# Performance work log

Hardware: AMD Instinct MI355X
Metric: run time of the kernel (lower is better)

Reference implementation:

```python
import jax, jax.numpy as jnp
import numpy as np

N = 50000
E = 800000
IN_CH = 64
HID = 128
K1 = 64
K2 = 16
THR = 1.0 / (K1 - 1)
EPS_LN = 1e-5


def setup_inputs() -> dict:
    key = jax.random.key(0)
    ks = jax.random.split(key, 10)
    def w(k, shape):
        return jax.random.normal(k, shape, jnp.float32) / np.sqrt(shape[0]).astype(np.float32)
    return {
        "x": jax.random.normal(ks[0], (N, IN_CH), jnp.float32),
        "edge_index": jax.random.randint(ks[1], (2, E), 0, N),
        "W1_rel": w(ks[2], (IN_CH, HID)),
        "b1_rel": jnp.zeros((HID,), jnp.float32),
        "W1_root": w(ks[3], (IN_CH, HID)),
        "Wp1": w(ks[4], (HID, K1)),
        "bp1": jnp.zeros((K1,), jnp.float32),
        "ln1_w": jnp.ones((K1,), jnp.float32),
        "ln1_b": jnp.zeros((K1,), jnp.float32),
        "W2_rel": w(ks[5], (HID, HID)),
        "b2_rel": jnp.zeros((HID,), jnp.float32),
        "W2_root": w(ks[6], (HID, HID)),
        "Wp2": w(ks[7], (HID, K2)),
        "bp2": jnp.zeros((K2,), jnp.float32),
        "ln2_w": jnp.ones((K2,), jnp.float32),
        "ln2_b": jnp.zeros((K2,), jnp.float32),
    }


def _layer_norm(x, w, b):
    m = x.mean(-1, keepdims=True)
    v = ((x - m) ** 2).mean(-1, keepdims=True)
    return (x - m) / jnp.sqrt(v + EPS_LN) * w + b


def _mincut_core(x, s, A_s, deg):
    # s already softmaxed. A_s[i] = sum_j A[i,j] s[j]; deg[i] = sum_j A[i,j].
    k = s.shape[1]
    pooled_x = s.T @ x                       # [k, F]
    pooled_adj = s.T @ A_s                   # [k, k]
    mincut_num = jnp.trace(pooled_adj)
    mincut_den = jnp.trace(s.T @ (deg[:, None] * s)) + 1e-10
    mincut_loss = -mincut_num / mincut_den
    sT_s = s.T @ s
    nrm = jnp.linalg.norm(sT_s)
    eye = jnp.eye(k, dtype=s.dtype)
    ortho_loss = jnp.linalg.norm(sT_s / (nrm + 1e-10) - eye / np.sqrt(k).astype(np.float32))
    adj = pooled_adj * (1.0 - eye)           # zero diagonal
    d_sqrt = jnp.sqrt(adj.sum(1))[:, None]
    inv = 1.0 / (d_sqrt + 1e-15)
    adj_norm = adj * inv * inv.T
    return pooled_x, adj_norm, mincut_loss, ortho_loss


def _forward(x, edge_index, W1_rel, b1_rel, W1_root, Wp1, bp1, ln1_w, ln1_b,
             W2_rel, b2_rel, W2_root, Wp2, bp2, ln2_w, ln2_b):
    n = x.shape[0]
    src, dst = edge_index[0], edge_index[1]
    # GraphConv 1: sum-aggregate source features at target, then linear + root
    agg1 = jax.ops.segment_sum(x[src], dst, num_segments=n)
    x1 = jax.nn.relu(agg1 @ W1_rel + b1_rel + x @ W1_root)
    s1 = _layer_norm(x1 @ Wp1 + bp1, ln1_w, ln1_b)
    s1_soft = jax.nn.softmax(s1, axis=-1)
    # sparse mincut pool 1 (edge list, unit weights): A_s[row] += s[col]
    A_s1 = jax.ops.segment_sum(s1_soft[src], src * 0 + src, num_segments=n) if False else jax.ops.segment_sum(s1_soft[dst], src, num_segments=n)
    deg1 = jax.ops.segment_sum(jnp.ones((E,), x.dtype), src, num_segments=n)
    x_pool1, adj1, mc1, o1 = _mincut_core(x1, s1_soft, A_s1, deg1)
    # threshold -> binary coarse adjacency (replaces torch nonzero edge list)
    A1 = jnp.where(adj1 > THR, 1.0, 0.0).astype(x.dtype)    # [K1, K1]
    # GraphConv 2 on dense binary A1 (edges (r,c): message x[r] -> node c)
    agg2 = A1.T @ x_pool1
    x2 = jax.nn.relu(agg2 @ W2_rel + b2_rel + x_pool1 @ W2_root)
    s2 = _layer_norm(x2 @ Wp2 + bp2, ln2_w, ln2_b)
    s2_soft = jax.nn.softmax(s2, axis=-1)
    A_s2 = A1 @ s2_soft
    deg2 = A1.sum(1)
    _, adj2, mc2, o2 = _mincut_core(x2, s2_soft, A_s2, deg2)
    return (mc1, o1, mc2, o2, s1, A1, s2, adj2)


def reference(x, edge_index, W1_rel, b1_rel, W1_root, Wp1, bp1, ln1_w, ln1_b,
              W2_rel, b2_rel, W2_root, Wp2, bp2, ln2_w, ln2_b):
    return _forward(x, edge_index, W1_rel, b1_rel, W1_root, Wp1, bp1, ln1_w, ln1_b,
                    W2_rel, b2_rel, W2_root, Wp2, bp2, ln2_w, ln2_b)
```

## Files before the change

kernel.cpp:

```cpp
#include <hip/hip_runtime.h>

#define NN 50000
#define EE 800000
#define NT32 1563
#define NTILE 3125
#define NSB 196
#define MAXSLAB 512

#define OUT_S1 4
#define OUT_A1 (4 + NN * 64)
#define OUT_S2 (OUT_A1 + 64 * 64)
#define OUT_ADJ2 (OUT_S2 + 64 * 16)

__device__ __forceinline__ float block_sum256(float v, float* red) {
  v += __shfl_xor(v, 32); v += __shfl_xor(v, 16); v += __shfl_xor(v, 8);
  v += __shfl_xor(v, 4);  v += __shfl_xor(v, 2);  v += __shfl_xor(v, 1);
  __syncthreads();
  if ((threadIdx.x & 63) == 0) red[threadIdx.x >> 6] = v;
  __syncthreads();
  return red[0] + red[1] + red[2] + red[3];
}

__device__ __forceinline__ float4 gather_rows64(
    const float* __restrict__ rows, const int* __restrict__ csr,
    int off, int c, int l, int g) {
  float4 a0 = make_float4(0.f, 0.f, 0.f, 0.f);
  float4 a1 = a0, a2 = a0, a3 = a0;
  int bb = 0;
  for (; bb + 16 <= c; bb += 16) {
    int myid = csr[off + bb + l];
    #pragma unroll
    for (int j = 0; j < 16; j += 4) {
      int s0 = __shfl(myid, g + j + 0, 64);
      int s1 = __shfl(myid, g + j + 1, 64);
      int s2 = __shfl(myid, g + j + 2, 64);
      int s3 = __shfl(myid, g + j + 3, 64);
      const float4 v0 = *(const float4*)&rows[(size_t)s0 * 64 + l * 4];
      const float4 v1 = *(const float4*)&rows[(size_t)s1 * 64 + l * 4];
      const float4 v2 = *(const float4*)&rows[(size_t)s2 * 64 + l * 4];
      const float4 v3 = *(const float4*)&rows[(size_t)s3 * 64 + l * 4];
      a0.x += v0.x; a0.y += v0.y; a0.z += v0.z; a0.w += v0.w;
      a1.x += v1.x; a1.y += v1.y; a1.z += v1.z; a1.w += v1.w;
      a2.x += v2.x; a2.y += v2.y; a2.z += v2.z; a2.w += v2.w;
      a3.x += v3.x; a3.y += v3.y; a3.z += v3.z; a3.w += v3.w;
    }
  }
  int m = c - bb;
  if (m > 0) {
    int myid = (l < m) ? csr[off + bb + l] : 0;
    int j = 0;
    for (; j + 2 <= m; j += 2) {
      int s0 = __shfl(myid, g + j + 0, 64);
      int s1 = __shfl(myid, g + j + 1, 64);
      const float4 v0 = *(const float4*)&rows[(size_t)s0 * 64 + l * 4];
      const float4 v1 = *(const float4*)&rows[(size_t)s1 * 64 + l * 4];
      a0.x += v0.x; a0.y += v0.y; a0.z += v0.z; a0.w += v0.w;
      a1.x += v1.x; a1.y += v1.y; a1.z += v1.z; a1.w += v1.w;
    }
    if (j < m) {
      int s0 = __shfl(myid, g + j, 64);
      const float4 v0 = *(const float4*)&rows[(size_t)s0 * 64 + l * 4];
      a2.x += v0.x; a2.y += v0.y; a2.z += v0.z; a2.w += v0.w;
    }
  }
  a0.x += a1.x; a0.y += a1.y; a0.z += a1.z; a0.w += a1.w;
  a2.x += a3.x; a2.y += a3.y; a2.z += a3.z; a2.w += a3.w;
  a0.x += a2.x; a0.y += a2.y; a0.z += a2.z; a0.w += a2.w;
  return a0;
}

__device__ __forceinline__ float4 gather_rows64_sq(
    const float* __restrict__ rows, const int* __restrict__ csr,
    int off, int c, int l, int g, float& dsq) {
  float4 a0 = make_float4(0.f, 0.f, 0.f, 0.f);
  float4 a1 = a0, a2 = a0, a3 = a0;
  int bb = 0;
  for (; bb + 16 <= c; bb += 16) {
    int myid = csr[off + bb + l];
    #pragma unroll
    for (int j = 0; j < 16; j += 4) {
      int s0 = __shfl(myid, g + j + 0, 64);
      int s1 = __shfl(myid, g + j + 1, 64);
      int s2 = __shfl(myid, g + j + 2, 64);
      int s3 = __shfl(myid, g + j + 3, 64);
      const float4 v0 = *(const float4*)&rows[(size_t)s0 * 64 + l * 4];
      const float4 v1 = *(const float4*)&rows[(size_t)s1 * 64 + l * 4];
      const float4 v2 = *(const float4*)&rows[(size_t)s2 * 64 + l * 4];
      const float4 v3 = *(const float4*)&rows[(size_t)s3 * 64 + l * 4];
      a0.x += v0.x; a0.y += v0.y; a0.z += v0.z; a0.w += v0.w;
      a1.x += v1.x; a1.y += v1.y; a1.z += v1.z; a1.w += v1.w;
      a2.x += v2.x; a2.y += v2.y; a2.z += v2.z; a2.w += v2.w;
      a3.x += v3.x; a3.y += v3.y; a3.z += v3.z; a3.w += v3.w;
      dsq += v0.x * v0.x + v0.y * v0.y + v0.z * v0.z + v0.w * v0.w;
      dsq += v1.x * v1.x + v1.y * v1.y + v1.z * v1.z + v1.w * v1.w;
      dsq += v2.x * v2.x + v2.y * v2.y + v2.z * v2.z + v2.w * v2.w;
      dsq += v3.x * v3.x + v3.y * v3.y + v3.z * v3.z + v3.w * v3.w;
    }
  }
  int m = c - bb;
  if (m > 0) {
    int myid = (l < m) ? csr[off + bb + l] : 0;
    int j = 0;
    for (; j + 2 <= m; j += 2) {
      int s0 = __shfl(myid, g + j + 0, 64);
      int s1 = __shfl(myid, g + j + 1, 64);
      const float4 v0 = *(const float4*)&rows[(size_t)s0 * 64 + l * 4];
      const float4 v1 = *(const float4*)&rows[(size_t)s1 * 64 + l * 4];
      a0.x += v0.x; a0.y += v0.y; a0.z += v0.z; a0.w += v0.w;
      a1.x += v1.x; a1.y += v1.y; a1.z += v1.z; a1.w += v1.w;
      dsq += v0.x * v0.x + v0.y * v0.y + v0.z * v0.z + v0.w * v0.w;
      dsq += v1.x * v1.x + v1.y * v1.y + v1.z * v1.z + v1.w * v1.w;
    }
    if (j < m) {
      int s0 = __shfl(myid, g + j, 64);
      const float4 v0 = *(const float4*)&rows[(size_t)s0 * 64 + l * 4];
      a2.x += v0.x; a2.y += v0.y; a2.z += v0.z; a2.w += v0.w;
      dsq += v0.x * v0.x + v0.y * v0.y + v0.z * v0.z + v0.w * v0.w;
    }
  }
  a0.x += a1.x; a0.y += a1.y; a0.z += a1.z; a0.w += a1.w;
  a2.x += a3.x; a2.y += a3.y; a2.z += a3.z; a2.w += a3.w;
  a0.x += a2.x; a0.y += a2.y; a0.z += a2.z; a0.w += a2.w;
  return a0;
}

__global__ __launch_bounds__(256) void k_hist(
    const int* __restrict__ ei, int* __restrict__ cnt_dst) {
  int e = blockIdx.x * 256 + threadIdx.x;
  int d = ei[EE + e];
  atomicAdd(&cnt_dst[d], 1);
}

__global__ __launch_bounds__(256) void k_scan1(
    const int* __restrict__ cnt, int* __restrict__ cursor, int* __restrict__ bsum) {
  __shared__ int sh[256];
  int t = threadIdx.x;
  int idx = blockIdx.x * 256 + t;
  int v = (idx < NN) ? cnt[idx] : 0;
  sh[t] = v;
  __syncthreads();
  for (int o = 1; o < 256; o <<= 1) {
    int u = (t >= o) ? sh[t - o] : 0;
    __syncthreads();
    sh[t] += u;
    __syncthreads();
  }
  if (idx < NN) cursor[idx] = sh[t] - v;
  if (t == 255) bsum[blockIdx.x] = sh[255];
}

__global__ __launch_bounds__(256) void k_scan2(
    int* __restrict__ bsum, float* __restrict__ den) {
  __shared__ int sh[256];
  int t = threadIdx.x;
  int v = (t < NSB) ? bsum[t] : 0;
  sh[t] = v;
  __syncthreads();
  for (int o = 1; o < 256; o <<= 1) {
    int u = (t >= o) ? sh[t - o] : 0;
    __syncthreads();
    sh[t] += u;
    __syncthreads();
  }
  if (t < NSB) bsum[t] = sh[t] - v;
  if (t == 0) den[0] = 0.f;
}

__global__ __launch_bounds__(256) void k_fill(
    const int* __restrict__ ei, int* __restrict__ cursor,
    const int* __restrict__ bsum, int* __restrict__ csr) {
  int e = blockIdx.x * 256 + threadIdx.x;
  int s = ei[e], d = ei[EE + e];
  int pos = atomicAdd(&cursor[d], 1) + bsum[d >> 8];
  csr[pos] = s;
}

__global__ __launch_bounds__(256, 4) void k_fused1(
    const float* __restrict__ x, const int* __restrict__ csr,
    const int* __restrict__ cur_end, const int* __restrict__ cnt,
    const int* __restrict__ bsum,
    const float* __restrict__ W1rel, const float* __restrict__ b1,
    const float* __restrict__ W1root,
    const float* __restrict__ Wp1, const float* __restrict__ bp1,
    const float* __restrict__ lnw, const float* __restrict__ lnb,
    float* __restrict__ x1, float* __restrict__ s1_out,
    float* __restrict__ s1s) {
  __shared__ float smem[4224];
  float* agg_t = smem;
  float* x_t   = smem + 2048;
  float* x1_t  = smem;
  int t = threadIdx.x;
  int base = blockIdx.x * 32;

  {
    int n16 = t >> 4, l = t & 15;
    #pragma unroll
    for (int half = 0; half < 2; ++half) {
      int n = n16 + half * 16;
      int node = base + n;
      if (node < NN) {
        *(float4*)&x_t[n * 64 + l * 4] = *(const float4*)&x[(size_t)node * 64 + l * 4];
        int c = cnt[node];
        int off = cur_end[node] - c + bsum[node >> 8];
        float4 acc = gather_rows64(x, csr, off, c, l, t & 48);
        *(float4*)&agg_t[n * 64 + l * 4] = acc;
      } else {
        float4 z = make_float4(0.f, 0.f, 0.f, 0.f);
        *(float4*)&x_t[n * 64 + l * 4] = z;
        *(float4*)&agg_t[n * 64 + l * 4] = z;
      }
    }
  }
  __syncthreads();

  int rg = t >> 5, cg = t & 31;
  int r0 = rg * 4;
  int c4 = cg * 4;
  float4 r0v, r1v, r2v, r3v;
  {
    float4 acc0 = *(const float4*)&b1[c4];
    float4 acc1 = acc0, acc2 = acc0, acc3 = acc0;
    #pragma unroll 4
    for (int k = 0; k < 64; ++k) {
      const float4 w1 = *(const float4*)&W1rel[k * 128 + c4];
      const float4 w2 = *(const float4*)&W1root[k * 128 + c4];
      float a0 = agg_t[(r0 + 0) * 64 + k], e0 = x_t[(r0 + 0) * 64 + k];
      float a1 = agg_t[(r0 + 1) * 64 + k], e1 = x_t[(r0 + 1) * 64 + k];
      float a2 = agg_t[(r0 + 2) * 64 + k], e2 = x_t[(r0 + 2) * 64 + k];
      float a3 = agg_t[(r0 + 3) * 64 + k], e3 = x_t[(r0 + 3) * 64 + k];
      acc0.x += a0 * w1.x + e0 * w2.x; acc0.y += a0 * w1.y + e0 * w2.y;
      acc0.z += a0 * w1.z + e0 * w2.z; acc0.w += a0 * w1.w + e0 * w2.w;
      acc1.x += a1 * w1.x + e1 * w2.x; acc1.y += a1 * w1.y + e1 * w2.y;
      acc1.z += a1 * w1.z + e1 * w2.z; acc1.w += a1 * w1.w + e1 * w2.w;
      acc2.x += a2 * w1.x + e2 * w2.x; acc2.y += a2 * w1.y + e2 * w2.y;
      acc2.z += a2 * w1.z + e2 * w2.z; acc2.w += a2 * w1.w + e2 * w2.w;
      acc3.x += a3 * w1.x + e3 * w2.x; acc3.y += a3 * w1.y + e3 * w2.y;
      acc3.z += a3 * w1.z + e3 * w2.z; acc3.w += a3 * w1.w + e3 * w2.w;
    }
    r0v.x = fmaxf(acc0.x, 0.f); r0v.y = fmaxf(acc0.y, 0.f);
    r0v.z = fmaxf(acc0.z, 0.f); r0v.w = fmaxf(acc0.w, 0.f);
    r1v.x = fmaxf(acc1.x, 0.f); r1v.y = fmaxf(acc1.y, 0.f);
    r1v.z = fmaxf(acc1.z, 0.f); r1v.w = fmaxf(acc1.w, 0.f);
    r2v.x = fmaxf(acc2.x, 0.f); r2v.y = fmaxf(acc2.y, 0.f);
    r2v.z = fmaxf(acc2.z, 0.f); r2v.w = fmaxf(acc2.w, 0.f);
    r3v.x = fmaxf(acc3.x, 0.f); r3v.y = fmaxf(acc3.y, 0.f);
    r3v.z = fmaxf(acc3.z, 0.f); r3v.w = fmaxf(acc3.w, 0.f);
    if (base + r0 + 3 < NN) {
      *(float4*)&x1[(size_t)(base + r0 + 0) * 128 + c4] = r0v;
      *(float4*)&x1[(size_t)(base + r0 + 1) * 128 + c4] = r1v;
      *(float4*)&x1[(size_t)(base + r0 + 2) * 128 + c4] = r2v;
      *(float4*)&x1[(size_t)(base + r0 + 3) * 128 + c4] = r3v;
    } else {
      if (base + r0 + 0 < NN) *(float4*)&x1[(size_t)(base + r0 + 0) * 128 + c4] = r0v;
      if (base + r0 + 1 < NN) *(float4*)&x1[(size_t)(base + r0 + 1) * 128 + c4] = r1v;
      if (base + r0 + 2 < NN) *(float4*)&x1[(size_t)(base + r0 + 2) * 128 + c4] = r2v;
    }
  }
  __syncthreads();
  *(float4*)&x1_t[(r0 + 0) * 132 + c4] = r0v;
  *(float4*)&x1_t[(r0 + 1) * 132 + c4] = r1v;
  *(float4*)&x1_t[(r0 + 2) * 132 + c4] = r2v;
  *(float4*)&x1_t[(r0 + 3) * 132 + c4] = r3v;
  __syncthreads();

  {
    int c2 = cg * 2;
    const float2 b0 = *(const float2*)&bp1[c2];
    float2 acc0 = b0, acc1 = b0, acc2 = b0, acc3 = b0;
    #pragma unroll 4
    for (int k0 = 0; k0 < 128; k0 += 4) {
      const float2 w0 = *(const float2*)&Wp1[(k0 + 0) * 64 + c2];
      const float2 w1 = *(const float2*)&Wp1[(k0 + 1) * 64 + c2];
      const float2 w2 = *(const float2*)&Wp1[(k0 + 2) * 64 + c2];
      const float2 w3 = *(const float2*)&Wp1[(k0 + 3) * 64 + c2];
      const float4 x0 = *(const float4*)&x1_t[(r0 + 0) * 132 + k0];
      const float4 x1v = *(const float4*)&x1_t[(r0 + 1) * 132 + k0];
      const float4 x2v = *(const float4*)&x1_t[(r0 + 2) * 132 + k0];
      const float4 x3v = *(const float4*)&x1_t[(r0 + 3) * 132 + k0];
      acc0.x += x0.x * w0.x + x0.y * w1.x + x0.z * w2.x + x0.w * w3.x;
      acc0.y += x0.x * w0.y + x0.y * w1.y + x0.z * w2.y + x0.w * w3.y;
      acc1.x += x1v.x * w0.x + x1v.y * w1.x + x1v.z * w2.x + x1v.w * w3.x;
      acc1.y += x1v.x * w0.y + x1v.y * w1.y + x1v.z * w2.y + x1v.w * w3.y;
      acc2.x += x2v.x * w0.x + x2v.y * w1.x + x2v.z * w2.x + x2v.w * w3.x;
      acc2.y += x2v.x * w0.y + x2v.y * w1.y + x2v.z * w2.y + x2v.w * w3.y;
      acc3.x += x3v.x * w0.x + x3v.y * w1.x + x3v.z * w2.x + x3v.w * w3.x;
      acc3.y += x3v.x * w0.y + x3v.y * w1.y + x3v.z * w2.y + x3v.w * w3.y;
    }
    const float2 lw = *(const float2*)&lnw[c2];
    const float2 lb = *(const float2*)&lnb[c2];
    float2 accs[4] = {acc0, acc1, acc2, acc3};
    #pragma unroll
    for (int i = 0; i < 4; ++i) {
      int row = base + r0 + i;
      float ax = accs[i].x, ay = accs[i].y;
      float m = ax + ay;
      m += __shfl_xor(m, 1); m += __shfl_xor(m, 2); m += __shfl_xor(m, 4);
      m += __shfl_xor(m, 8); m += __shfl_xor(m, 16);
      m *= (1.0f / 64.0f);
      float dx = ax - m, dy = ay - m;
      float v = dx * dx + dy * dy;
      v += __shfl_xor(v, 1); v += __shfl_xor(v, 2); v += __shfl_xor(v, 4);
      v += __shfl_xor(v, 8); v += __shfl_xor(v, 16);
      v *= (1.0f / 64.0f);
      float rstd = rsqrtf(v + 1e-5f);
      float lnx = dx * rstd * lw.x + lb.x;
      float lny = dy * rstd * lw.y + lb.y;
      float mx = fmaxf(lnx, lny);
      mx = fmaxf(mx, __shfl_xor(mx, 1)); mx = fmaxf(mx, __shfl_xor(mx, 2));
      mx = fmaxf(mx, __shfl_xor(mx, 4)); mx = fmaxf(mx, __shfl_xor(mx, 8));
      mx = fmaxf(mx, __shfl_xor(mx, 16));
      float ex = expf(lnx - mx), ey = expf(lny - mx);
      float se = ex + ey;
      se += __shfl_xor(se, 1); se += __shfl_xor(se, 2); se += __shfl_xor(se, 4);
      se += __shfl_xor(se, 8); se += __shfl_xor(se, 16);
      float inv = 1.0f / se;
      ex *= inv; ey *= inv;
      if (row < NN) {
        *(float2*)&s1_out[(size_t)row * 64 + c2] = make_float2(lnx, lny);
        *(float2*)&s1s[(size_t)row * 64 + c2] = make_float2(ex, ey);
      }
    }
  }
}

__global__ __launch_bounds__(256, 4) void k_pooled_all(
    const float* __restrict__ s1s, const float* __restrict__ x1,
    const int* __restrict__ csr, const int* __restrict__ cur_end,
    const int* __restrict__ cnt, const int* __restrict__ bsum,
    float* __restrict__ part, float* __restrict__ den) {
  __shared__ float s_t[1024];
  __shared__ float g_t[1024];
  __shared__ float x_t[2048];
  __shared__ float red[4];
  int t = threadIdx.x;
  int kg = t >> 5;
  int cg = t & 31;
  int c1 = cg * 4;
  int cc = (cg & 15) * 4;
  bool is_padj = (cg < 16);
  float a1[8][4], a2[8][4];
  float dsq = 0.f;
  #pragma unroll
  for (int j = 0; j < 8; ++j)
    #pragma unroll
    for (int q = 0; q < 4; ++q) { a1[j][q] = 0.f; a2[j][q] = 0.f; }

  for (int tile = blockIdx.x; tile < NTILE; tile += gridDim.x) {
    size_t base = (size_t)tile * 16;
    __syncthreads();
    *(float4*)&s_t[t * 4] = *(const float4*)&s1s[base * 64 + t * 4];
    *(float4*)&x_t[t * 8] = *(const float4*)&x1[base * 128 + t * 8];
    *(float4*)&x_t[t * 8 + 4] = *(const float4*)&x1[base * 128 + t * 8 + 4];
    {
      int n16 = t >> 4, l = t & 15;
      int node = (int)base + n16;
      int c = cnt[node];
      int off = cur_end[node] - c + bsum[node >> 8];
      float4 acc = gather_rows64_sq(s1s, csr, off, c, l, t & 48, dsq);
      *(float4*)&g_t[n16 * 64 + l * 4] = acc;
    }
    __syncthreads();
    #pragma unroll 2
    for (int r = 0; r < 16; ++r) {
      const float4 xv = *(const float4*)&x_t[r * 128 + c1];
      const float4 sv = *(const float4*)&s_t[r * 64 + cc];
      const float4 k0 = *(const float4*)&s_t[r * 64 + kg * 8];
      const float4 k1 = *(const float4*)&s_t[r * 64 + kg * 8 + 4];
      const float4 g0 = *(const float4*)&g_t[r * 64 + kg * 8];
      const float4 g1 = *(const float4*)&g_t[r * 64 + kg * 8 + 4];
      float sk[8] = {k0.x, k0.y, k0.z, k0.w, k1.x, k1.y, k1.z, k1.w};
      float gk[8] = {g0.x, g0.y, g0.z, g0.w, g1.x, g1.y, g1.z, g1.w};
      #pragma unroll
      for (int j = 0; j < 8; ++j) {
        float m2 = is_padj ? gk[j] : sk[j];
        a1[j][0] += sk[j] * xv.x; a1[j][1] += sk[j] * xv.y;
        a1[j][2] += sk[j] * xv.z; a1[j][3] += sk[j] * xv.w;
        a2[j][0] += m2 * sv.x; a2[j][1] += m2 * sv.y;
        a2[j][2] += m2 * sv.z; a2[j][3] += m2 * sv.w;
      }
    }
  }
  float* slab = part + (size_t)blockIdx.x * 16384;
  float* o2base = slab + (is_padj ? 8192 : 12288);
  #pragma unroll
  for (int j = 0; j < 8; ++j) {
    int k = kg * 8 + j;
    *(float4*)&slab[k * 128 + c1] = make_float4(a1[j][0], a1[j][1], a1[j][2], a1[j][3]);
    *(float4*)&o2base[k * 64 + cc] = make_float4(a2[j][0], a2[j][1], a2[j][2], a2[j][3]);
  }
  float dtot = block_sum256(dsq, red);
  if (t == 0) atomicAdd(den, dtot);
}

__global__ __launch_bounds__(256) void k_reduce1(
    const float* __restrict__ part, int nslab, int chunk,
    float* __restrict__ part2) {
  int ib = blockIdx.x & 15;
  int bs = blockIdx.x >> 4;
  int i4 = ib * 256 + threadIdx.x;
  int b0 = bs * chunk;
  int b1 = b0 + chunk; if (b1 > nslab) b1 = nslab;
  float4 acc = make_float4(0.f, 0.f, 0.f, 0.f);
  for (int b = b0; b < b1; ++b) {
    const float4 v = *(const float4*)&part[(size_t)b * 16384 + (size_t)i4 * 4];
    acc.x += v.x; acc.y += v.y; acc.z += v.z; acc.w += v.w;
  }
  *(float4*)&part2[(size_t)bs * 16384 + (size_t)i4 * 4] = acc;
}

__global__ __launch_bounds__(256) void k_reduce2(
    const float* __restrict__ part2, float* __restrict__ dst) {
  int i = blockIdx.x * 256 + threadIdx.x;
  float acc = 0.f;
  #pragma unroll
  for (int b = 0; b < 32; ++b) acc += part2[b * 16384 + i];
  dst[i] = acc;
}

__global__ __launch_bounds__(256) void k_p2a(
    const float* __restrict__ padj_g, const float* __restrict__ sts_g,
    const float* __restrict__ den_g, const float* __restrict__ px_g,
    float* __restrict__ out, float* __restrict__ A1f, float* __restrict__ agg2) {
  __shared__ float padj[4096];
  __shared__ float A1s[4096];
  __shared__ float invs[64];
  __shared__ float red[4];
  int t = threadIdx.x;
  for (int i = t; i < 4096; i += 256) padj[i] = padj_g[i];
  __syncthreads();
  float num = (t < 64) ? padj[t * 64 + t] : 0.f;
  num = block_sum256(num, red);
  float n2 = 0.f;
  for (int i = t; i < 4096; i += 256) { float v = sts_g[i]; n2 += v * v; }
  n2 = block_sum256(n2, red);
  float nrm = sqrtf(n2);
  float oacc = 0.f;
  for (int i = t; i < 4096; i += 256) {
    float v = sts_g[i] / (nrm + 1e-10f);
    if ((i >> 6) == (i & 63)) v -= 0.125f;
    oacc += v * v;
  }
  oacc = block_sum256(oacc, red);
  if (t == 0) {
    out[0] = -num / (den_g[0] + 1e-10f);
    out[1] = sqrtf(oacc);
  }
  if (t < 64) {
    float rs = 0.f;
    for (int j = 0; j < 64; ++j)
      if (j != t) rs += padj[t * 64 + j];
    invs[t] = 1.0f / (sqrtf(rs) + 1e-15f);
  }
  __syncthreads();
  const float THRv = 1.0f / 63.0f;
  for (int i = t; i < 4096; i += 256) {
    int r = i >> 6, c = i & 63;
    float a = (r == c) ? 0.f : padj[i] * invs[r] * invs[c];
    float b = (a > THRv) ? 1.0f : 0.0f;
    out[OUT_A1 + i] = b;
    A1f[i] = b;
    A1s[i] = b;
  }
  __syncthreads();
  int j = t >> 2, q = t & 3;
  float acc[32];
  #pragma unroll
  for (int c = 0; c < 32; ++c) acc[c] = 0.f;
  for (int i = 0; i < 64; ++i) {
    float a = A1s[i * 64 + j];
    const float* pxr = px_g + i * 128 + q * 32;
    #pragma unroll
    for (int c = 0; c < 32; ++c) acc[c] += a * pxr[c];
  }
  #pragma unroll
  for (int c = 0; c < 32; ++c) agg2[j * 128 + q * 32 + c] = acc[c];
}

__global__ __launch_bounds__(128) void k_x2(
    const float* __restrict__ agg2, const float* __restrict__ px,
    const float* __restrict__ W2rel, const float* __restrict__ b2,
    const float* __restrict__ W2root, float* __restrict__ x2) {
  int row = blockIdx.x, col = threadIdx.x;
  const float* ar = agg2 + row * 128;
  const float* xr = px + row * 128;
  float acc = b2[col];
  #pragma unroll 4
  for (int k = 0; k < 128; ++k)
    acc += ar[k] * W2rel[k * 128 + col] + xr[k] * W2root[k * 128 + col];
  x2[row * 128 + col] = fmaxf(acc, 0.f);
}

__global__ __launch_bounds__(256) void k_p2c(
    const float* __restrict__ x2g, const float* __restrict__ Wp2,
    const float* __restrict__ bp2, const float* __restrict__ lnw,
    const float* __restrict__ lnb, const float* __restrict__ A1f,
    float* __restrict__ out) {
  __shared__ float A1s[4096];
  __shared__ float s2lin[1024];
  __shared__ float s2s[1024];
  __shared__ float As2[1024];
  __shared__ float deg2[64];
  __shared__ float padj2[256];
  __shared__ float sts2[256];
  __shared__ float inv2[16];
  __shared__ float red[4];
  int t = threadIdx.x;
  for (int i = t; i < 4096; i += 256) A1s[i] = A1f[i];
  for (int it = 0; it < 4; ++it) {
    int idx = t + it * 256;
    int r = idx >> 4, c = idx & 15;
    float acc = bp2[c];
    const float* xr = x2g + r * 128;
    #pragma unroll 8
    for (int k = 0; k < 128; ++k) acc += xr[k] * Wp2[k * 16 + c];
    s2lin[idx] = acc;
  }
  __syncthreads();
  if (t < 64) {
    float m = 0.f;
    #pragma unroll
    for (int c = 0; c < 16; ++c) m += s2lin[t * 16 + c];
    m *= (1.0f / 16.0f);
    float v = 0.f;
    #pragma unroll
    for (int c = 0; c < 16; ++c) { float d = s2lin[t * 16 + c] - m; v += d * d; }
    v *= (1.0f / 16.0f);
    float rstd = rsqrtf(v + 1e-5f);
    float mx = -1e30f;
    float lnv[16];
    #pragma unroll
    for (int c = 0; c < 16; ++c) {
      lnv[c] = (s2lin[t * 16 + c] - m) * rstd * lnw[c] + lnb[c];
      out[OUT_S2 + t * 16 + c] = lnv[c];
      mx = fmaxf(mx, lnv[c]);
    }
    float se = 0.f;
    #pragma unroll
    for (int c = 0; c < 16; ++c) { float e = expf(lnv[c] - mx); s2s[t * 16 + c] = e; se += e; }
    float inv = 1.0f / se;
    #pragma unroll
    for (int c = 0; c < 16; ++c) s2s[t * 16 + c] *= inv;
    float dg = 0.f;
    for (int j = 0; j < 64; ++j) dg += A1s[t * 64 + j];
    deg2[t] = dg;
  }
  __syncthreads();
  for (int it = 0; it < 4; ++it) {
    int idx = t + it * 256;
    int i = idx >> 4, c = idx & 15;
    float acc = 0.f;
    for (int j = 0; j < 64; ++j) acc += A1s[i * 64 + j] * s2s[j * 16 + c];
    As2[idx] = acc;
  }
  __syncthreads();
  {
    int a = t >> 4, b = t & 15;
    float acc = 0.f, accs = 0.f;
    for (int i = 0; i < 64; ++i) {
      float sa = s2s[i * 16 + a];
      acc += sa * As2[i * 16 + b];
      accs += sa * s2s[i * 16 + b];
    }
    padj2[t] = acc;
    sts2[t] = accs;
  }
  __syncthreads();
  float num2 = (t < 16) ? padj2[t * 17] : 0.f;
  num2 = block_sum256(num2, red);
  float dpart = 0.f;
  if (t < 64) {
    float ss = 0.f;
    #pragma unroll
    for (int c = 0; c < 16; ++c) ss += s2s[t * 16 + c] * s2s[t * 16 + c];
    dpart = deg2[t] * ss;
  }
  float den2 = block_sum256(dpart, red);
  float n2 = sts2[t] * sts2[t];
  n2 = block_sum256(n2, red);
  float nrm2 = sqrtf(n2);
  float ov;
  {
    float v = sts2[t] / (nrm2 + 1e-10f);
    if ((t >> 4) == (t & 15)) v -= 0.25f;
    ov = v * v;
  }
  ov = block_sum256(ov, red);
  if (t == 0) {
    out[2] = -num2 / (den2 + 1e-10f);
    out[3] = sqrtf(ov);
  }
  if (t < 16) {
    float rs = 0.f;
    #pragma unroll
    for (int b = 0; b < 16; ++b)
      if (b != t) rs += padj2[t * 16 + b];
    inv2[t] = 1.0f / (sqrtf(rs) + 1e-15f);
  }
  __syncthreads();
  {
    int a = t >> 4, b = t & 15;
    float v = (a == b) ? 0.f : padj2[t] * inv2[a] * inv2[b];
    out[OUT_ADJ2 + t] = v;
  }
}

extern "C" void kernel_launch(void* const* d_in, const int* in_sizes, int n_in,
                              void* d_out, int out_size, void* d_ws, size_t ws_size,
                              hipStream_t stream) {
  const float* x      = (const float*)d_in[0];
  const int*   ei     = (const int*)d_in[1];
  const float* W1_rel = (const float*)d_in[2];
  const float* b1_rel = (const float*)d_in[3];
  const float* W1_root= (const float*)d_in[4];
  const float* Wp1    = (const float*)d_in[5];
  const float* bp1    = (const float*)d_in[6];
  const float* ln1w   = (const float*)d_in[7];
  const float* ln1b   = (const float*)d_in[8];
  const float* W2_rel = (const float*)d_in[9];
  const float* b2_rel = (const float*)d_in[10];
  const float* W2_root= (const float*)d_in[11];
  const float* Wp2    = (const float*)d_in[12];
  const float* bp2    = (const float*)d_in[13];
  const float* ln2w   = (const float*)d_in[14];
  const float* ln2b   = (const float*)d_in[15];
  float* out = (float*)d_out;

  int* cnt_dst = (int*)d_ws;
  int* cursor  = cnt_dst + NN;
  int* bsum    = cursor + NN;
  int* csr     = bsum + 256;
  float* x1    = (float*)(csr + EE);
  float* s1s   = x1 + (size_t)NN * 128;
  float* dst   = s1s + (size_t)NN * 64;
  float* px    = dst;
  float* padj  = dst + 8192;
  float* sts   = dst + 12288;
  float* den   = dst + 16384;
  float* A1f   = den + 4;
  float* agg2  = A1f + 4096;
  float* x2    = agg2 + 8192;
  float* part2 = x2 + 8192;
  float* part  = part2 + 32 * 16384;

  size_t used_floats = (size_t)(part - (float*)d_ws);
  size_t avail = ws_size / 4 - used_floats;
  int nslab = (int)(avail / 16384);
  if (nslab > MAXSLAB) nslab = MAXSLAB;
  if (nslab < 1) nslab = 1;
  int chunk = (nslab + 31) / 32;

  hipMemsetAsync(cnt_dst, 0, NN * sizeof(int), stream);

  k_hist<<<EE / 256, 256, 0, stream>>>(ei, cnt_dst);
  k_scan1<<<NSB, 256, 0, stream>>>(cnt_dst, cursor, bsum);
  k_scan2<<<1, 256, 0, stream>>>(bsum, den);
  k_fill<<<EE / 256, 256, 0, stream>>>(ei, cursor, bsum, csr);
  k_fused1<<<NT32, 256, 0, stream>>>(x, csr, cursor, cnt_dst, bsum,
                                     W1_rel, b1_rel, W1_root, Wp1, bp1,
                                     ln1w, ln1b, x1, out + OUT_S1, s1s);
  k_pooled_all<<<nslab, 256, 0, stream>>>(s1s, x1, csr, cursor, cnt_dst, bsum,
                                          part, den);
  k_reduce1<<<512, 256, 0, stream>>>(part, nslab, chunk, part2);
  k_reduce2<<<64, 256, 0, stream>>>(part2, dst);
  k_p2a<<<1, 256, 0, stream>>>(padj, sts, den, px, out, A1f, agg2);
  k_x2<<<64, 128, 0, stream>>>(agg2, px, W2_rel, b2_rel, W2_root, x2);
  k_p2c<<<1, 256, 0, stream>>>(x2, Wp2, bp2, ln2w, ln2b, A1f, out);
}
```

Baseline: 416.2 us.

## Bucket CSR neighbor lists by source range within each destination

The CSR build now histograms edges into four buckets per destination node, keyed by which quarter of the node range the source falls in. Neighbor lists are therefore partly sorted by source index, which should improve locality of the row gathers. k_pooled_all walks the four buckets as separate gathers, while k_fused1 gathers the whole concatenated span. The cost is a 4x larger count and scan array, a wider second scan pass, and more per-node index loads.

After: 439.0 us. 1.05x slower.

```diff
diff --git a/kernel.cpp b/kernel.cpp
--- a/kernel.cpp
+++ b/kernel.cpp
@@ -4,7 +4,9 @@
 #define EE 800000
 #define NT32 1563
 #define NTILE 3125
-#define NSB 196
+#define RNG 12500
+#define N4 200000
+#define NSB1 782
 #define MAXSLAB 512
 
 #define OUT_S1 4
@@ -125,10 +127,10 @@
 }
 
 __global__ __launch_bounds__(256) void k_hist(
-    const int* __restrict__ ei, int* __restrict__ cnt_dst) {
+    const int* __restrict__ ei, int* __restrict__ cnt4) {
   int e = blockIdx.x * 256 + threadIdx.x;
-  int d = ei[EE + e];
-  atomicAdd(&cnt_dst[d], 1);
+  int s = ei[e], d = ei[EE + e];
+  atomicAdd(&cnt4[d * 4 + s / RNG], 1);
 }
 
 __global__ __launch_bounds__(256) void k_scan1(
@@ -136,7 +138,7 @@
   __shared__ int sh[256];
   int t = threadIdx.x;
   int idx = blockIdx.x * 256 + t;
-  int v = (idx < NN) ? cnt[idx] : 0;
+  int v = (idx < N4) ? cnt[idx] : 0;
   sh[t] = v;
   __syncthreads();
   for (int o = 1; o < 256; o <<= 1) {
@@ -145,24 +147,24 @@
     sh[t] += u;
     __syncthreads();
   }
-  if (idx < NN) cursor[idx] = sh[t] - v;
+  if (idx < N4) cursor[idx] = sh[t] - v;
   if (t == 255) bsum[blockIdx.x] = sh[255];
 }
 
-__global__ __launch_bounds__(256) void k_scan2(
+__global__ __launch_bounds__(1024) void k_scan2(
     int* __restrict__ bsum, float* __restrict__ den) {
-  __shared__ int sh[256];
+  __shared__ int sh[1024];
   int t = threadIdx.x;
-  int v = (t < NSB) ? bsum[t] : 0;
+  int v = (t < NSB1) ? bsum[t] : 0;
   sh[t] = v;
   __syncthreads();
-  for (int o = 1; o < 256; o <<= 1) {
+  for (int o = 1; o < 1024; o <<= 1) {
     int u = (t >= o) ? sh[t - o] : 0;
     __syncthreads();
     sh[t] += u;
     __syncthreads();
   }
-  if (t < NSB) bsum[t] = sh[t] - v;
+  if (t < NSB1) bsum[t] = sh[t] - v;
   if (t == 0) den[0] = 0.f;
 }
 
@@ -171,13 +173,14 @@
     const int* __restrict__ bsum, int* __restrict__ csr) {
   int e = blockIdx.x * 256 + threadIdx.x;
   int s = ei[e], d = ei[EE + e];
-  int pos = atomicAdd(&cursor[d], 1) + bsum[d >> 8];
+  int idx = d * 4 + s / RNG;
+  int pos = atomicAdd(&cursor[idx], 1) + bsum[idx >> 8];
   csr[pos] = s;
 }
 
 __global__ __launch_bounds__(256, 4) void k_fused1(
     const float* __restrict__ x, const int* __restrict__ csr,
-    const int* __restrict__ cur_end, const int* __restrict__ cnt,
+    const int* __restrict__ cur4, const int* __restrict__ cnt4,
     const int* __restrict__ bsum,
     const float* __restrict__ W1rel, const float* __restrict__ b1,
     const float* __restrict__ W1root,
@@ -200,9 +203,10 @@
       int node = base + n;
       if (node < NN) {
         *(float4*)&x_t[n * 64 + l * 4] = *(const float4*)&x[(size_t)node * 64 + l * 4];
-        int c = cnt[node];
-        int off = cur_end[node] - c + bsum[node >> 8];
-        float4 acc = gather_rows64(x, csr, off, c, l, t & 48);
+        int nb = node * 4;
+        int c0 = cnt4[nb], c1 = cnt4[nb + 1], c2 = cnt4[nb + 2], c3 = cnt4[nb + 3];
+        int off = cur4[nb] - c0 + bsum[nb >> 8];
+        float4 acc = gather_rows64(x, csr, off, c0 + c1 + c2 + c3, l, t & 48);
         *(float4*)&agg_t[n * 64 + l * 4] = acc;
       } else {
         float4 z = make_float4(0.f, 0.f, 0.f, 0.f);
@@ -325,8 +329,8 @@
 
 __global__ __launch_bounds__(256, 4) void k_pooled_all(
     const float* __restrict__ s1s, const float* __restrict__ x1,
-    const int* __restrict__ csr, const int* __restrict__ cur_end,
-    const int* __restrict__ cnt, const int* __restrict__ bsum,
+    const int* __restrict__ csr, const int* __restrict__ cur4,
+    const int* __restrict__ cnt4, const int* __restrict__ bsum,
     float* __restrict__ part, float* __restrict__ den) {
   __shared__ float s_t[1024];
   __shared__ float g_t[1024];
@@ -354,9 +358,14 @@
     {
       int n16 = t >> 4, l = t & 15;
       int node = (int)base + n16;
-      int c = cnt[node];
-      int off = cur_end[node] - c + bsum[node >> 8];
-      float4 acc = gather_rows64_sq(s1s, csr, off, c, l, t & 48, dsq);
+      int nb = node * 4;
+      float4 acc = make_float4(0.f, 0.f, 0.f, 0.f);
+      for (int r = 0; r < 4; ++r) {
+        int c = cnt4[nb + r];
+        int off = cur4[nb + r] - c + bsum[(nb + r) >> 8];
+        float4 gsum = gather_rows64_sq(s1s, csr, off, c, l, t & 48, dsq);
+        acc.x += gsum.x; acc.y += gsum.y; acc.z += gsum.z; acc.w += gsum.w;
+      }
       *(float4*)&g_t[n16 * 64 + l * 4] = acc;
     }
     __syncthreads();
@@ -625,10 +634,10 @@
   const float* ln2b   = (const float*)d_in[15];
   float* out = (float*)d_out;
 
-  int* cnt_dst = (int*)d_ws;
-  int* cursor  = cnt_dst + NN;
-  int* bsum    = cursor + NN;
-  int* csr     = bsum + 256;
+  int* cnt4    = (int*)d_ws;
+  int* cursor4 = cnt4 + N4;
+  int* bsum    = cursor4 + N4;
+  int* csr     = bsum + 1024;
   float* x1    = (float*)(csr + EE);
   float* s1s   = x1 + (size_t)NN * 128;
   float* dst   = s1s + (size_t)NN * 64;
@@ -649,16 +658,16 @@
   if (nslab < 1) nslab = 1;
   int chunk = (nslab + 31) / 32;
 
-  hipMemsetAsync(cnt_dst, 0, NN * sizeof(int), stream);
-
-  k_hist<<<EE / 256, 256, 0, stream>>>(ei, cnt_dst);
-  k_scan1<<<NSB, 256, 0, stream>>>(cnt_dst, cursor, bsum);
-  k_scan2<<<1, 256, 0, stream>>>(bsum, den);
-  k_fill<<<EE / 256, 256, 0, stream>>>(ei, cursor, bsum, csr);
-  k_fused1<<<NT32, 256, 0, stream>>>(x, csr, cursor, cnt_dst, bsum,
+  hipMemsetAsync(cnt4, 0, N4 * sizeof(int), stream);
+
+  k_hist<<<EE / 256, 256, 0, stream>>>(ei, cnt4);
+  k_scan1<<<NSB1, 256, 0, stream>>>(cnt4, cursor4, bsum);
+  k_scan2<<<1, 1024, 0, stream>>>(bsum, den);
+  k_fill<<<EE / 256, 256, 0, stream>>>(ei, cursor4, bsum, csr);
+  k_fused1<<<NT32, 256, 0, stream>>>(x, csr, cursor4, cnt4, bsum,
                                      W1_rel, b1_rel, W1_root, Wp1, bp1,
                                      ln1w, ln1b, x1, out + OUT_S1, s1s);
-  k_pooled_all<<<nslab, 256, 0, stream>>>(s1s, x1, csr, cursor, cnt_dst, bsum,
+  k_pooled_all<<<nslab, 256, 0, stream>>>(s1s, x1, csr, cursor4, cnt4, bsum,
                                           part, den);
   k_reduce1<<<512, 256, 0, stream>>>(part, nslab, chunk, part2);
   k_reduce2<<<64, 256, 0, stream>>>(part2, dst);
```
